# Kernel tuning notes

Hardware: AMD Instinct MI355X
Metric: run time of the kernel (lower is better)

Reference implementation:

```python
import jax, jax.numpy as jnp
import numpy as np

START_LABEL_ID = 4  # tag_to_ix['[CLS]']


def setup_inputs() -> dict:
    key = jax.random.key(0)
    k1, k2 = jax.random.split(key)
    B, T, K = 256, 4096, 6
    feats = jax.random.normal(k1, (B, T, K), dtype=jnp.float32)
    transitions = jax.random.normal(k2, (B, T, K, K), dtype=jnp.float32)
    return {"feats": feats, "transitions": transitions}


def reference(feats, transitions):
    # Viterbi decode (Bert_BiLSTM_CRF._viterbi_decode):
    #   log_delta init -10000 except start tag; per step t:
    #     scores   = transitions[:, t] + log_delta[:, None, :]   # [B, K, K]
    #     log_delta = max_k scores + feats[:, t]
    #     psi[:, t] = argmax_k scores  (backpointers)
    B, T, K = feats.shape
    init = jnp.full((B, K), -10000.0, dtype=feats.dtype).at[:, START_LABEL_ID].set(0.0)

    def step(delta, xs):
        trans_t, feat_t = xs                       # [B,K,K], [B,K]
        scores = trans_t + delta[:, None, :]       # [B,K,K]
        new_delta = jnp.max(scores, axis=-1) + feat_t
        psi_t = jnp.argmax(scores, axis=-1)        # [B,K] backpointers
        return new_delta, psi_t

    # time-major xs for scan over t = 1..T-1
    xs = (jnp.swapaxes(transitions[:, 1:], 0, 1),  # [T-1,B,K,K]
          jnp.swapaxes(feats[:, 1:], 0, 1))        # [T-1,B,K]
    final_delta, psis = jax.lax.scan(step, init, xs)  # psis: [T-1,B,K]

    score = jnp.max(final_delta, axis=-1)              # [B]
    last_tag = jnp.argmax(final_delta, axis=-1)        # [B]

    # Backtrack: path[t] = psi[t+1][path[t+1]]; psis[i] is psi at time i+1,
    # so path[t] = gather(psis[t], path[t+1]) for t = T-2 .. 0.
    def back(next_tag, psi_t):
        tag = jnp.take_along_axis(psi_t, next_tag[:, None], axis=-1)[:, 0]
        return tag, tag

    _, tags = jax.lax.scan(back, last_tag, psis, reverse=True)  # tags[i] = path[i], i=0..T-2
    path = jnp.concatenate([tags, last_tag[None, :]], axis=0).T  # [B,T]
    return score, path
```

## Files before the change

### kernel.cpp

```cpp
#include <hip/hip_runtime.h>

#define NB 256
#define NT 4096
#define CH 128
#define NCHUNK (NT / CH)

typedef unsigned int u32;
typedef unsigned long long u64;
typedef int v2i __attribute__((ext_vector_type(2)));

typedef __attribute__((address_space(1))) const u32 gas_u32;
typedef __attribute__((address_space(3))) u32 las_u32;

__device__ __forceinline__ void gll16(const void* g, void* l) {
  __builtin_amdgcn_global_load_lds((gas_u32*)g, (las_u32*)l, 16, 0, 0);
}

template <int CTRL>
__device__ __forceinline__ float dppf(float x) {
  return __int_as_float(__builtin_amdgcn_update_dpp(
      0, __float_as_int(x), CTRL, 0xF, 0xF, true));
}

__device__ __forceinline__ float pl16max(float x) {
#if __has_builtin(__builtin_amdgcn_permlane16_swap)
  v2i r = __builtin_amdgcn_permlane16_swap(__float_as_int(x), __float_as_int(x),
                                           false, false);
  return fmaxf(__int_as_float(r[0]), __int_as_float(r[1]));
#else
  return fmaxf(x, __shfl_xor(x, 16, 64));
#endif
}

__device__ __forceinline__ float pl32max(float x) {
#if __has_builtin(__builtin_amdgcn_permlane32_swap)
  v2i r = __builtin_amdgcn_permlane32_swap(__float_as_int(x), __float_as_int(x),
                                           false, false);
  return fmaxf(__int_as_float(r[0]), __int_as_float(r[1]));
#else
  return fmaxf(x, __shfl_xor(x, 32, 64));
#endif
}

__global__ void __launch_bounds__(64, 1)
viterbi_k(const float* __restrict__ feats, const float* __restrict__ trans,
          float* __restrict__ out) {
  __shared__ __align__(16) float s_tr[2 * CH * 36];
  __shared__ __align__(16) float s_ft[2 * CH * 6];
  __shared__ u32 s_psi[NT];
  __shared__ u32 s_path[NT / 4];

  const int b = blockIdx.x;
  const int lane = (int)threadIdx.x;
  const int g = lane >> 3;
  const int l = lane & 7;
  const int gg = (g < 6) ? g : 5;
  const int jj = (l < 6) ? l : 5;
  const int offTA = gg * 6 + jj;
  const int offTB = jj * 6 + gg;
  const int offFA = gg;
  const int offFB = jj;

  const float* trb = trans + (size_t)b * NT * 36;
  const float* ftb = feats + (size_t)b * NT * 6;

  float delta = (l == 4) ? 0.0f : -10000.0f;
  u32 mlo = 0, mhi = 0;

  auto stage = [&](int c) {
    const int buf = c & 1;
    const float* gt = trb + (size_t)c * CH * 36;
    float* lt = s_tr + buf * (CH * 36);
#pragma unroll
    for (int i = 0; i < 18; ++i) gll16(gt + i * 256 + lane * 4, lt + i * 256);
    const float* gf = ftb + (size_t)c * CH * 6;
    float* lf = s_ft + buf * (CH * 6);
#pragma unroll
    for (int i = 0; i < 3; ++i) gll16(gf + i * 256 + lane * 4, lf + i * 256);
  };

  auto stepA = [&](float tr, float ft, int slot) {
    float s = tr + delta;
    float m = fmaxf(s, dppf<0xB1>(s));
    m = fmaxf(m, dppf<0x4E>(m));
    m = fmaxf(m, dppf<0x141>(m));
    u64 bal = __ballot(s == m);
    bool cap = (lane == slot);
    mlo = cap ? (u32)bal : mlo;
    mhi = cap ? (u32)(bal >> 32) : mhi;
    delta = m + ft;
  };

  auto stepB = [&](float tr, float ft, int slot) {
    float s = tr + delta;
    float m = fmaxf(s, dppf<0x128>(s));
    m = pl16max(m);
    m = pl32max(m);
    u64 bal = __ballot(s == m);
    bool cap = (lane == slot);
    mlo = cap ? (u32)bal : mlo;
    mhi = cap ? (u32)(bal >> 32) : mhi;
    delta = m + ft;
  };

  auto flush = [&](int base) {
    const u32 ub = (u32)(base >> 6) & 63;
    u32 pA = (u32)__builtin_ctz((mlo & 63u) | 64u);
    pA |= (u32)__builtin_ctz(((mlo >> 8) & 63u) | 64u) << 3;
    pA |= (u32)__builtin_ctz(((mlo >> 16) & 63u) | 64u) << 6;
    pA |= (u32)__builtin_ctz(((mlo >> 24) & 63u) | 64u) << 9;
    pA |= (u32)__builtin_ctz((mhi & 63u) | 64u) << 12;
    pA |= (u32)__builtin_ctz(((mhi >> 8) & 63u) | 64u) << 15;
    u64 bal = ((u64)mhi << 32) | (u64)mlo;
    u32 pB = 0;
#pragma unroll
    for (int i = 0; i < 6; ++i) {
      u64 mm = (bal >> i) & 0x0000010101010101ULL;
      u32 j = (u32)(__builtin_ctzll(mm | (1ULL << 48)) >> 3);
      pB |= j << (3 * i);
    }
    u32 p = (lane & 1) ? pA : pB;
    s_psi[base + (((u32)lane) ^ ub)] = p;
  };

#define LOAD8(trv, ftv, g8base)                                               \
  {                                                                           \
    _Pragma("unroll") for (int q = 0; q < 8; ++q) {                           \
      trv[q] = trp[((g8base) + q) * 36 + ((q & 1) ? offTA : offTB)];          \
      ftv[q] = ftp[((g8base) + q) * 6 + ((q & 1) ? offFA : offFB)];           \
    }                                                                         \
  }

#define STEPS8L(trv, ftv, base, ntr, nft, ng8)                                \
  {                                                                           \
    _Pragma("unroll") for (int q = 0; q < 8; ++q) {                           \
      if (q & 1) stepA(trv[q], ftv[q], ((base) + q) & 63);                    \
      else       stepB(trv[q], ftv[q], ((base) + q) & 63);                    \
      ntr[q] = trp[((ng8) + q) * 36 + ((q & 1) ? offTA : offTB)];             \
      nft[q] = ftp[((ng8) + q) * 6 + ((q & 1) ? offFA : offFB)];              \
    }                                                                         \
  }

#define STEPS8(trv, ftv, base)                                                \
  {                                                                           \
    _Pragma("unroll") for (int q = 0; q < 8; ++q) {                           \
      if (q & 1) stepA(trv[q], ftv[q], ((base) + q) & 63);                    \
      else       stepB(trv[q], ftv[q], ((base) + q) & 63);                    \
    }                                                                         \
  }

  stage(0);
  asm volatile("s_waitcnt vmcnt(0)" ::: "memory");
  stage(1);

  {
    const float* trp = s_tr;
    const float* ftp = s_ft;
    float trA[8], ftA[8], trB[8], ftB[8];
    LOAD8(trA, ftA, 0);
    LOAD8(trB, ftB, 8);
#pragma unroll
    for (int q = 1; q < 8; ++q) {
      if (q & 1) stepA(trA[q], ftA[q], q);
      else       stepB(trA[q], ftA[q], q);
    }
    STEPS8L(trB, ftB, 8, trA, ftA, 16);
#pragma unroll 1
    for (int g2 = 2; g2 < 14; g2 += 2) {
      STEPS8L(trA, ftA, g2 * 8, trB, ftB, (g2 + 1) * 8);
      STEPS8L(trB, ftB, (g2 + 1) * 8, trA, ftA, (g2 + 2) * 8);
      if ((g2 & 7) == 6) flush((g2 & 8) * 8);
    }
    STEPS8L(trA, ftA, 112, trB, ftB, 120);
    STEPS8(trB, ftB, 120);
    flush(64);
  }

#pragma unroll 1
  for (int c = 1; c < NCHUNK; ++c) {
    asm volatile("s_waitcnt vmcnt(0)" ::: "memory");
    if (c + 1 < NCHUNK) stage(c + 1);
    const int buf = c & 1;
    const float* trp = s_tr + buf * (CH * 36);
    const float* ftp = s_ft + buf * (CH * 6);
    const int tbase = c * CH;
    float trA[8], ftA[8], trB[8], ftB[8];
    LOAD8(trA, ftA, 0);
#pragma unroll 1
    for (int g2 = 0; g2 < 14; g2 += 2) {
      STEPS8L(trA, ftA, tbase + g2 * 8, trB, ftB, (g2 + 1) * 8);
      STEPS8L(trB, ftB, tbase + (g2 + 1) * 8, trA, ftA, (g2 + 2) * 8);
      if ((g2 & 7) == 6) flush(tbase + (g2 & 8) * 8);
    }
    STEPS8L(trA, ftA, tbase + 112, trB, ftB, 120);
    STEPS8(trB, ftB, tbase + 120);
    flush(tbase + 64);
  }

  float sm = delta;
  sm = fmaxf(sm, dppf<0xB1>(sm));
  sm = fmaxf(sm, dppf<0x4E>(sm));
  sm = fmaxf(sm, dppf<0x141>(sm));
  sm = fmaxf(sm, dppf<0x128>(sm));
  sm = pl16max(sm);
  sm = pl32max(sm);
  u64 bs = __ballot(delta == sm);
  int last_tag = (int)((__builtin_ctzll(bs) >> 3) & 7);

  __syncthreads();

  const int u = lane;
  u32 Gm = 0u | (1u << 3) | (2u << 6) | (3u << 9) | (4u << 12) | (5u << 15);
#pragma unroll 1
  for (int k = 0; k < 64; ++k) {
    u32 p = s_psi[u * 64 + (k ^ u)];
    u32 ng = 0;
#pragma unroll
    for (int x = 0; x < 6; ++x) {
      u32 j = (p >> (3 * x)) & 7;
      u32 v = (Gm >> (3 * ((j < 6) ? j : 0))) & 7;
      ng |= v << (3 * x);
    }
    Gm = ng;
  }

  int bcur = last_tag;
  int my_b = last_tag;
#pragma unroll 1
  for (int v = 63; v >= 1; --v) {
    u32 Gv = (u32)__builtin_amdgcn_readlane((int)Gm, v);
    bcur = (int)((Gv >> (3 * bcur)) & 7);
    my_b = (u == v - 1) ? bcur : my_b;
  }

  {
    int tag = my_b;
    unsigned char* pb = (unsigned char*)s_path;
    pb[u * 64 + 63] = (unsigned char)tag;
#pragma unroll 1
    for (int k = 63; k >= 1; --k) {
      u32 p = s_psi[u * 64 + (k ^ u)];
      tag = (int)((p >> (3 * tag)) & 7);
      pb[u * 64 + k - 1] = (unsigned char)tag;
    }
  }
  if (lane == 0) out[b] = sm;
  __syncthreads();

  float* outp = out + NB + (size_t)b * NT;
#pragma unroll
  for (int i = 0; i < (NT / 4) / 64; ++i) {
    u32 w = s_path[lane + i * 64];
    float4 f;
    f.x = (float)(w & 255u);
    f.y = (float)((w >> 8) & 255u);
    f.z = (float)((w >> 16) & 255u);
    f.w = (float)((w >> 24) & 255u);
    ((float4*)outp)[lane + i * 64] = f;
  }
}

extern "C" void kernel_launch(void* const* d_in, const int* in_sizes, int n_in,
                              void* d_out, int out_size, void* d_ws, size_t ws_size,
                              hipStream_t stream) {
  (void)in_sizes; (void)n_in; (void)out_size; (void)d_ws; (void)ws_size;
  const float* feats = (const float*)d_in[0];
  const float* trans = (const float*)d_in[1];
  float* out = (float*)d_out;
  hipLaunchKernelGGL(viterbi_k, dim3(NB), dim3(64), 0, stream, feats, trans, out);
}
```

Measured before the change: 240.1 us.

## Pack eight batch waves per block, spill backpointers to global output

Each block now runs eight independent waves, one batch row each, instead of a single wave. To fit them in LDS, the chunk size drops to 16 steps with per-wave double buffers. Backpointers are written to the output buffer in global memory rather than LDS, then reloaded into registers for the backtrack, and the path is packed and stored without LDS. The aim is higher per-CU occupancy, hiding latency on the serial recurrence. The cost is more frequent small staging waits and extra global traffic for the backpointers, whose reuse of the output region is only safe because each wave overwrites its own psi area with the path after reading it.

```diff
diff --git a/kernel.cpp b/kernel.cpp
--- a/kernel.cpp
+++ b/kernel.cpp
@@ -2,8 +2,8 @@
 
 #define NB 256
 #define NT 4096
-#define CH 128
-#define NCHUNK (NT / CH)
+#define CH 16
+#define W 8
 
 typedef unsigned int u32;
 typedef unsigned long long u64;
@@ -42,16 +42,15 @@
 #endif
 }
 
-__global__ void __launch_bounds__(64, 1)
+__global__ void __launch_bounds__(512, 2)
 viterbi_k(const float* __restrict__ feats, const float* __restrict__ trans,
           float* __restrict__ out) {
-  __shared__ __align__(16) float s_tr[2 * CH * 36];
-  __shared__ __align__(16) float s_ft[2 * CH * 6];
-  __shared__ u32 s_psi[NT];
-  __shared__ u32 s_path[NT / 4];
-
-  const int b = blockIdx.x;
-  const int lane = (int)threadIdx.x;
+  __shared__ __align__(16) float s_tr[W * 2 * CH * 36];
+  __shared__ __align__(16) float s_ft[W * 2 * CH * 6];
+
+  const int wave = (int)(threadIdx.x >> 6);
+  const int lane = (int)(threadIdx.x & 63);
+  const int b = blockIdx.x * W + wave;
   const int g = lane >> 3;
   const int l = lane & 7;
   const int gg = (g < 6) ? g : 5;
@@ -63,20 +62,24 @@
 
   const float* trb = trans + (size_t)b * NT * 36;
   const float* ftb = feats + (size_t)b * NT * 6;
+  u32* psig = (u32*)out + NB + (size_t)b * NT;
+
+  float* trsl = s_tr + wave * (2 * CH * 36);
+  float* ftsl = s_ft + wave * (2 * CH * 6);
 
   float delta = (l == 4) ? 0.0f : -10000.0f;
   u32 mlo = 0, mhi = 0;
 
   auto stage = [&](int c) {
     const int buf = c & 1;
-    const float* gt = trb + (size_t)c * CH * 36;
-    float* lt = s_tr + buf * (CH * 36);
-#pragma unroll
-    for (int i = 0; i < 18; ++i) gll16(gt + i * 256 + lane * 4, lt + i * 256);
-    const float* gf = ftb + (size_t)c * CH * 6;
-    float* lf = s_ft + buf * (CH * 6);
-#pragma unroll
-    for (int i = 0; i < 3; ++i) gll16(gf + i * 256 + lane * 4, lf + i * 256);
+    const float* gt = trb + (size_t)c * (CH * 36);
+    float* lt = trsl + buf * (CH * 36);
+    gll16(gt + lane * 4, lt);
+    gll16(gt + 256 + lane * 4, lt + 256);
+    if (lane < 16) gll16(gt + 512 + lane * 4, lt + 512);
+    const float* gf = ftb + (size_t)c * (CH * 6);
+    float* lf = ftsl + buf * (CH * 6);
+    if (lane < 24) gll16(gf + lane * 4, lf);
   };
 
   auto stepA = [&](float tr, float ft, int slot) {
@@ -104,7 +107,6 @@
   };
 
   auto flush = [&](int base) {
-    const u32 ub = (u32)(base >> 6) & 63;
     u32 pA = (u32)__builtin_ctz((mlo & 63u) | 64u);
     pA |= (u32)__builtin_ctz(((mlo >> 8) & 63u) | 64u) << 3;
     pA |= (u32)__builtin_ctz(((mlo >> 16) & 63u) | 64u) << 6;
@@ -120,7 +122,7 @@
       pB |= j << (3 * i);
     }
     u32 p = (lane & 1) ? pA : pB;
-    s_psi[base + (((u32)lane) ^ ub)] = p;
+    psig[base + lane] = p;
   };
 
 #define LOAD8(trv, ftv, g8base)                                               \
@@ -153,48 +155,67 @@
   asm volatile("s_waitcnt vmcnt(0)" ::: "memory");
   stage(1);
 
-  {
-    const float* trp = s_tr;
-    const float* ftp = s_ft;
-    float trA[8], ftA[8], trB[8], ftB[8];
-    LOAD8(trA, ftA, 0);
-    LOAD8(trB, ftB, 8);
-#pragma unroll
-    for (int q = 1; q < 8; ++q) {
-      if (q & 1) stepA(trA[q], ftA[q], q);
-      else       stepB(trA[q], ftA[q], q);
-    }
-    STEPS8L(trB, ftB, 8, trA, ftA, 16);
+  const float* trp;
+  const float* ftp;
+  float trA[8], ftA[8], trB[8], ftB[8];
+
+  trp = trsl; ftp = ftsl;
+  LOAD8(trA, ftA, 0);
+  LOAD8(trB, ftB, 8);
+#pragma unroll
+  for (int q = 1; q < 8; ++q) {
+    if (q & 1) stepA(trA[q], ftA[q], q);
+    else       stepB(trA[q], ftA[q], q);
+  }
+  STEPS8(trB, ftB, 8);
+  asm volatile("s_waitcnt vmcnt(0)" ::: "memory");
+  stage(2);
+  trp = trsl + CH * 36; ftp = ftsl + CH * 6;
+  LOAD8(trA, ftA, 0);
+  STEPS8L(trA, ftA, 16, trB, ftB, 8);
+  STEPS8(trB, ftB, 24);
+  asm volatile("s_waitcnt vmcnt(0)" ::: "memory");
+  stage(3);
+  trp = trsl; ftp = ftsl;
+  LOAD8(trA, ftA, 0);
+  STEPS8L(trA, ftA, 32, trB, ftB, 8);
+  STEPS8(trB, ftB, 40);
+  asm volatile("s_waitcnt vmcnt(0)" ::: "memory");
+  stage(4);
+  trp = trsl + CH * 36; ftp = ftsl + CH * 6;
+  LOAD8(trA, ftA, 0);
+  STEPS8L(trA, ftA, 48, trB, ftB, 8);
+  STEPS8(trB, ftB, 56);
+  flush(0);
+
 #pragma unroll 1
-    for (int g2 = 2; g2 < 14; g2 += 2) {
-      STEPS8L(trA, ftA, g2 * 8, trB, ftB, (g2 + 1) * 8);
-      STEPS8L(trB, ftB, (g2 + 1) * 8, trA, ftA, (g2 + 2) * 8);
-      if ((g2 & 7) == 6) flush((g2 & 8) * 8);
-    }
-    STEPS8L(trA, ftA, 112, trB, ftB, 120);
-    STEPS8(trB, ftB, 120);
-    flush(64);
-  }
-
-#pragma unroll 1
-  for (int c = 1; c < NCHUNK; ++c) {
+  for (int w = 1; w < 64; ++w) {
+    const int tb = w * 64;
+    asm volatile("s_waitcnt vmcnt(1)" ::: "memory");
+    stage(4 * w + 1);
+    trp = trsl; ftp = ftsl;
+    LOAD8(trA, ftA, 0);
+    STEPS8L(trA, ftA, tb, trB, ftB, 8);
+    STEPS8(trB, ftB, tb + 8);
     asm volatile("s_waitcnt vmcnt(0)" ::: "memory");
-    if (c + 1 < NCHUNK) stage(c + 1);
-    const int buf = c & 1;
-    const float* trp = s_tr + buf * (CH * 36);
-    const float* ftp = s_ft + buf * (CH * 6);
-    const int tbase = c * CH;
-    float trA[8], ftA[8], trB[8], ftB[8];
-    LOAD8(trA, ftA, 0);
-#pragma unroll 1
-    for (int g2 = 0; g2 < 14; g2 += 2) {
-      STEPS8L(trA, ftA, tbase + g2 * 8, trB, ftB, (g2 + 1) * 8);
-      STEPS8L(trB, ftB, tbase + (g2 + 1) * 8, trA, ftA, (g2 + 2) * 8);
-      if ((g2 & 7) == 6) flush(tbase + (g2 & 8) * 8);
-    }
-    STEPS8L(trA, ftA, tbase + 112, trB, ftB, 120);
-    STEPS8(trB, ftB, tbase + 120);
-    flush(tbase + 64);
+    stage(4 * w + 2);
+    trp = trsl + CH * 36; ftp = ftsl + CH * 6;
+    LOAD8(trA, ftA, 0);
+    STEPS8L(trA, ftA, tb + 16, trB, ftB, 8);
+    STEPS8(trB, ftB, tb + 24);
+    asm volatile("s_waitcnt vmcnt(0)" ::: "memory");
+    stage(4 * w + 3);
+    trp = trsl; ftp = ftsl;
+    LOAD8(trA, ftA, 0);
+    STEPS8L(trA, ftA, tb + 32, trB, ftB, 8);
+    STEPS8(trB, ftB, tb + 40);
+    asm volatile("s_waitcnt vmcnt(0)" ::: "memory");
+    if (w < 63) stage(4 * w + 4);
+    trp = trsl + CH * 36; ftp = ftsl + CH * 6;
+    LOAD8(trA, ftA, 0);
+    STEPS8L(trA, ftA, tb + 48, trB, ftB, 8);
+    STEPS8(trB, ftB, tb + 56);
+    flush(tb);
   }
 
   float sm = delta;
@@ -207,18 +228,20 @@
   u64 bs = __ballot(delta == sm);
   int last_tag = (int)((__builtin_ctzll(bs) >> 3) & 7);
 
-  __syncthreads();
-
-  const int u = lane;
+  asm volatile("s_waitcnt vmcnt(0)" ::: "memory");
+  u32 p[64];
+#pragma unroll
+  for (int k = 0; k < 64; ++k) p[k] = psig[lane * 64 + k];
+
   u32 Gm = 0u | (1u << 3) | (2u << 6) | (3u << 9) | (4u << 12) | (5u << 15);
-#pragma unroll 1
+#pragma unroll
   for (int k = 0; k < 64; ++k) {
-    u32 p = s_psi[u * 64 + (k ^ u)];
+    u32 pp = p[k];
     u32 ng = 0;
 #pragma unroll
     for (int x = 0; x < 6; ++x) {
-      u32 j = (p >> (3 * x)) & 7;
-      u32 v = (Gm >> (3 * ((j < 6) ? j : 0))) & 7;
+      u32 j = (pp >> (3 * x)) & 7;
+      u32 v = (Gm >> (3 * j)) & 7;
       ng |= v << (3 * x);
     }
     Gm = ng;
@@ -230,33 +253,32 @@
   for (int v = 63; v >= 1; --v) {
     u32 Gv = (u32)__builtin_amdgcn_readlane((int)Gm, v);
     bcur = (int)((Gv >> (3 * bcur)) & 7);
-    my_b = (u == v - 1) ? bcur : my_b;
-  }
-
-  {
-    int tag = my_b;
-    unsigned char* pb = (unsigned char*)s_path;
-    pb[u * 64 + 63] = (unsigned char)tag;
-#pragma unroll 1
-    for (int k = 63; k >= 1; --k) {
-      u32 p = s_psi[u * 64 + (k ^ u)];
-      tag = (int)((p >> (3 * tag)) & 7);
-      pb[u * 64 + k - 1] = (unsigned char)tag;
-    }
-  }
+    my_b = (lane == v - 1) ? bcur : my_b;
+  }
+
+  u32 pw[16];
+#pragma unroll
+  for (int i = 0; i < 16; ++i) pw[i] = 0;
+  int tag = my_b;
+  pw[15] = (u32)tag << 24;
+#pragma unroll
+  for (int k = 63; k >= 1; --k) {
+    tag = (int)((p[k] >> (3 * tag)) & 7);
+    pw[(k - 1) >> 2] |= (u32)tag << (8 * ((k - 1) & 3));
+  }
+
   if (lane == 0) out[b] = sm;
-  __syncthreads();
 
   float* outp = out + NB + (size_t)b * NT;
 #pragma unroll
-  for (int i = 0; i < (NT / 4) / 64; ++i) {
-    u32 w = s_path[lane + i * 64];
+  for (int i = 0; i < 16; ++i) {
+    u32 wd = pw[i];
     float4 f;
-    f.x = (float)(w & 255u);
-    f.y = (float)((w >> 8) & 255u);
-    f.z = (float)((w >> 16) & 255u);
-    f.w = (float)((w >> 24) & 255u);
-    ((float4*)outp)[lane + i * 64] = f;
+    f.x = (float)(wd & 255u);
+    f.y = (float)((wd >> 8) & 255u);
+    f.z = (float)((wd >> 16) & 255u);
+    f.w = (float)((wd >> 24) & 255u);
+    *(float4*)(outp + (size_t)(lane * 16 + i) * 4) = f;
   }
 }
 
@@ -267,5 +289,6 @@
   const float* feats = (const float*)d_in[0];
   const float* trans = (const float*)d_in[1];
   float* out = (float*)d_out;
-  hipLaunchKernelGGL(viterbi_k, dim3(NB), dim3(64), 0, stream, feats, trans, out);
-}
+  hipLaunchKernelGGL(viterbi_k, dim3(NB / W), dim3(64 * W), 0, stream,
+                     feats, trans, out);
+}
```

Result: slower. 395.2 us (+64.6%).
